# Kernel optimization log

Hardware: AMD Instinct MI355X
Metric: run time of the kernel (lower is better)

Reference implementation:

```python
import jax, jax.numpy as jnp
import numpy as np

T = 100.0  # temperature, from init_kwargs
B = 4096
D = 128
NUM_CLASSES = 10


def setup_inputs() -> dict:
    key = jax.random.key(0)
    kx, ky = jax.random.split(key)
    x = jax.random.normal(kx, (B, D), dtype=jnp.float32)
    y = jax.random.randint(ky, (B,), 0, NUM_CLASSES, dtype=jnp.int64)
    return {"x": x, "y": y}


def reference(x, y):
    # Pairwise squared Euclidean distances: dist[i,j] = ||x_i - x_j||^2
    sq = jnp.sum(x * x, axis=1)                      # [b]
    dist = sq[:, None] + sq[None, :] - 2.0 * (x @ x.T)  # [b, b]
    dist = jnp.maximum(dist, 0.0)                    # clamp fp error; diag -> 0

    e = jnp.exp(-dist / T)                           # [b, b]; e[i,i] = 1

    b = x.shape[0]
    same = (y[:, None] == y[None, :])                # same-label mask
    not_self = ~jnp.eye(b, dtype=bool)

    # numerator: sum over j != i with y[j] == y[i]
    num = jnp.sum(jnp.where(same & not_self, e, 0.0), axis=1)  # [b]
    # denominator: sum over ALL j, including j == i (exp(0) = 1), as in the
    # original loop where the denominator accumulates unconditionally
    den = jnp.sum(e, axis=1)                         # [b]

    return jnp.mean(-jnp.log(num / den))
```

## Files before the change

kernel.cpp:

```cpp
#include <hip/hip_runtime.h>
#include <hip/hip_bf16.h>

#define NB 4096

typedef short v8s __attribute__((ext_vector_type(8)));
typedef float v4f __attribute__((ext_vector_type(4)));


__global__ __launch_bounds__(256) void prep_kernel(const float* __restrict__ x,
        float* __restrict__ sq, unsigned short* __restrict__ xb,
        float* __restrict__ out) {
    int tid = threadIdx.x;
    int row = blockIdx.x * 8 + (tid >> 5);
    int lane = tid & 31;
    const float4* xg = (const float4*)x;
    float4 v = xg[row * 32 + lane];
    __hip_bfloat16 h0 = __float2bfloat16(v.x), h1 = __float2bfloat16(v.y);
    __hip_bfloat16 h2 = __float2bfloat16(v.z), h3 = __float2bfloat16(v.w);
    ushort4 u4;
    u4.x = *(unsigned short*)&h0; u4.y = *(unsigned short*)&h1;
    u4.z = *(unsigned short*)&h2; u4.w = *(unsigned short*)&h3;
    ((ushort4*)xb)[row * 32 + lane] = u4;
    float f0 = __bfloat162float(h0), f1 = __bfloat162float(h1);
    float f2 = __bfloat162float(h2), f3 = __bfloat162float(h3);
    float s = f0 * f0 + f1 * f1 + f2 * f2 + f3 * f3;
    #pragma unroll
    for (int off = 16; off > 0; off >>= 1) s += __shfl_down(s, off);
    if (lane == 0) sq[row] = s;
    if (blockIdx.x == 0 && tid == 0) out[0] = 0.f;
}

__global__ __launch_bounds__(256) void snn_mfma(const unsigned short* __restrict__ xb,
        const int* __restrict__ y, const float* __restrict__ sqg,
        float2* __restrict__ part) {
    __shared__ __align__(16) union {
        unsigned short tiles[2 * 128 * 136];
        float part[2 * 128 * 34];
    } sm;
    __shared__ float sqi[128], sqj[128];
    __shared__ int yi[128], yj[128];
    float2* partC = (float2*)&sm.part[2 * 128 * 34];

    const int tid = threadIdx.x;
    const int wave = tid >> 6;
    const int lane = tid & 63;
    const int wm = wave >> 1;
    const int wn = wave & 1;
    const int lr = lane & 15;
    const int q  = lane >> 4;

    int t = blockIdx.x;
    int by = (int)((sqrtf(8.0f * (float)t + 1.0f) - 1.0f) * 0.5f);
    if (by * (by + 1) / 2 > t) --by;
    if ((by + 1) * (by + 2) / 2 <= t) ++by;
    int bx = t - by * (by + 1) / 2;
    const int i0 = bx * 128;
    const int j0 = by * 128;
    const bool offdiag = (bx != by);

    unsigned short* At = sm.tiles;
    unsigned short* Bt = sm.tiles + 128 * 136;
    const v8s* xg = (const v8s*)xb;

    #pragma unroll
    for (int r = 0; r < 8; ++r) {
        int c = r * 256 + tid;
        int row = c >> 4, cc = c & 15;
        *(v8s*)&At[row * 136 + cc * 8] = xg[(i0 + row) * 16 + cc];
        *(v8s*)&Bt[row * 136 + cc * 8] = xg[(j0 + row) * 16 + cc];
    }
    if (tid < 128) { sqi[tid] = sqg[i0 + tid]; yi[tid] = y[i0 + tid]; }
    else { sqj[tid - 128] = sqg[j0 + tid - 128]; yj[tid - 128] = y[j0 + tid - 128]; }
    __syncthreads();

    v4f acc[4][4];
    #pragma unroll
    for (int mt = 0; mt < 4; ++mt)
        #pragma unroll
        for (int nt = 0; nt < 4; ++nt)
            #pragma unroll
            for (int r = 0; r < 4; ++r) acc[mt][nt][r] = 0.f;

    #pragma unroll
    for (int kk = 0; kk < 4; ++kk) {
        v8s af[4], bf[4];
        #pragma unroll
        for (int mt = 0; mt < 4; ++mt)
            af[mt] = *(const v8s*)&At[(wm * 64 + mt * 16 + lr) * 136 + kk * 32 + q * 8];
        #pragma unroll
        for (int nt = 0; nt < 4; ++nt)
            bf[nt] = *(const v8s*)&Bt[(wn * 64 + nt * 16 + lr) * 136 + kk * 32 + q * 8];
        #pragma unroll
        for (int mt = 0; mt < 4; ++mt)
            #pragma unroll
            for (int nt = 0; nt < 4; ++nt)
                acc[mt][nt] = __builtin_amdgcn_mfma_f32_16x16x32_bf16(
                    af[mt], bf[nt], acc[mt][nt], 0, 0, 0);
    }

    __syncthreads();

    float sqj_r[4]; int yj_r[4], jg[4];
    #pragma unroll
    for (int nt = 0; nt < 4; ++nt) {
        int jc = wn * 64 + nt * 16 + lr;
        sqj_r[nt] = sqj[jc]; yj_r[nt] = yj[jc]; jg[nt] = j0 + jc;
    }
    float colN[4] = {0.f, 0.f, 0.f, 0.f};
    float colD[4] = {0.f, 0.f, 0.f, 0.f};

    #pragma unroll
    for (int mt = 0; mt < 4; ++mt) {
        #pragma unroll
        for (int r = 0; r < 4; ++r) {
            int rloc = wm * 64 + mt * 16 + q * 4 + r;
            float si = sqi[rloc]; int yir = yi[rloc]; int ig = i0 + rloc;
            float n = 0.f, d = 0.f;
            #pragma unroll
            for (int nt = 0; nt < 4; ++nt) {
                float dist = fmaxf(si + sqj_r[nt] - 2.f * acc[mt][nt][r], 0.f);
                float e = __builtin_amdgcn_exp2f(dist * -0.014426950408889634f);
                d += e;
                bool ok = (yir == yj_r[nt]) && (ig != jg[nt]);
                float ne = ok ? e : 0.f;
                n += ne;
                colN[nt] += ne;
                colD[nt] += e;
            }
            *(float2*)&sm.part[((wn * 128 + rloc) * 17 + lr) * 2] = make_float2(n, d);
        }
    }
    if (offdiag) {
        #pragma unroll
        for (int nt = 0; nt < 4; ++nt) {
            float cn = colN[nt], cd = colD[nt];
            cn += __shfl_xor(cn, 16); cd += __shfl_xor(cd, 16);
            cn += __shfl_xor(cn, 32); cd += __shfl_xor(cd, 32);
            if (q == 0) partC[wm * 128 + wn * 64 + nt * 16 + lr] = make_float2(cn, cd);
        }
    }
    __syncthreads();

    {
        int row = tid >> 1, h = tid & 1;
        const float2* p = (const float2*)&sm.part[(h * 128 + row) * 34];
        float sn = 0.f, sd = 0.f;
        #pragma unroll
        for (int c = 0; c < 16; ++c) { float2 v = p[c]; sn += v.x; sd += v.y; }
        sn += __shfl_down(sn, 1); sd += __shfl_down(sd, 1);
        if (h == 0) part[(i0 + row) * 32 + by] = make_float2(sn, sd);
    }
    if (offdiag && tid < 128) {
        float2 a = partC[tid], b = partC[128 + tid];
        part[(j0 + tid) * 32 + bx] = make_float2(a.x + b.x, a.y + b.y);
    }
}

__global__ __launch_bounds__(256) void snn_final(const float2* __restrict__ part,
        float* __restrict__ out) {
    __shared__ float wsum[4];
    int row = blockIdx.x * 256 + threadIdx.x;
    const float4* p = (const float4*)&part[row * 32];
    float n = 0.f, d = 0.f;
    #pragma unroll
    for (int c = 0; c < 16; ++c) {
        float4 v = p[c];
        n += v.x + v.z; d += v.y + v.w;
    }
    float l = __logf(d) - __logf(n);
    #pragma unroll
    for (int off = 32; off > 0; off >>= 1) l += __shfl_down(l, off);
    int wid = threadIdx.x >> 6;
    if ((threadIdx.x & 63) == 0) wsum[wid] = l;
    __syncthreads();
    if (threadIdx.x == 0) {
        float s = wsum[0] + wsum[1] + wsum[2] + wsum[3];
        atomicAdd(out, s * (1.0f / NB));
    }
}

extern "C" void kernel_launch(void* const* d_in, const int* in_sizes, int n_in,
                              void* d_out, int out_size, void* d_ws, size_t ws_size,
                              hipStream_t stream) {
    const float* x = (const float*)d_in[0];
    const int*   y = (const int*)d_in[1];
    float* out = (float*)d_out;
    float2* part = (float2*)d_ws;
    float* sq = (float*)((char*)d_ws + (1 << 20));
    unsigned short* xb = (unsigned short*)((char*)d_ws + (1 << 20) + (16 << 10));

    prep_kernel<<<NB / 8, 256, 0, stream>>>(x, sq, xb, out);
    snn_mfma<<<528, 256, 0, stream>>>(xb, y, sq, part);
    snn_final<<<NB / 256, 256, 0, stream>>>(part, out);
}
```

Baseline: 72.34 us.

## Stage bf16 slabs via global_load_lds double buffering with k-major layout

The prep kernel now writes the bf16 copy of x in a k-chunk-major transposed layout. The MFMA kernel streams A/B k-slabs straight into LDS with global_load_lds, double-buffered so the next slab loads while the current one is multiplied. Row partial sums are now reduced with wave shuffles instead of a padded LDS scratch, which shrinks shared memory. A minimum-occupancy hint is added to launch bounds. This adds per-k barriers, and correctness relies on those barriers waiting for the async LDS loads.

```diff
diff --git a/kernel.cpp b/kernel.cpp
--- a/kernel.cpp
+++ b/kernel.cpp
@@ -7,8 +7,14 @@
 typedef float v4f __attribute__((ext_vector_type(4)));
 
 
+__device__ __forceinline__ void dma16(const unsigned short* g, unsigned short* l) {
+    __builtin_amdgcn_global_load_lds(
+        (const __attribute__((address_space(1))) unsigned int*)g,
+        (__attribute__((address_space(3))) unsigned int*)l, 16, 0, 0);
+}
+
 __global__ __launch_bounds__(256) void prep_kernel(const float* __restrict__ x,
-        float* __restrict__ sq, unsigned short* __restrict__ xb,
+        float* __restrict__ sq, unsigned short* __restrict__ xbT,
         float* __restrict__ out) {
     int tid = threadIdx.x;
     int row = blockIdx.x * 8 + (tid >> 5);
@@ -20,7 +26,8 @@
     ushort4 u4;
     u4.x = *(unsigned short*)&h0; u4.y = *(unsigned short*)&h1;
     u4.z = *(unsigned short*)&h2; u4.w = *(unsigned short*)&h3;
-    ((ushort4*)xb)[row * 32 + lane] = u4;
+    int c = lane >> 1, half = lane & 1;
+    *(ushort4*)&xbT[((size_t)c * 4096 + row) * 8 + half * 4] = u4;
     float f0 = __bfloat162float(h0), f1 = __bfloat162float(h1);
     float f2 = __bfloat162float(h2), f3 = __bfloat162float(h3);
     float s = f0 * f0 + f1 * f1 + f2 * f2 + f3 * f3;
@@ -30,22 +37,21 @@
     if (blockIdx.x == 0 && tid == 0) out[0] = 0.f;
 }
 
-__global__ __launch_bounds__(256) void snn_mfma(const unsigned short* __restrict__ xb,
+__global__ __launch_bounds__(256, 4) void snn_mfma(const unsigned short* __restrict__ xbT,
         const int* __restrict__ y, const float* __restrict__ sqg,
         float2* __restrict__ part) {
     __shared__ __align__(16) union {
-        unsigned short tiles[2 * 128 * 136];
-        float part[2 * 128 * 34];
+        unsigned short slab[2][2][4][128][8];
+        float2 red[4][128];
     } sm;
     __shared__ float sqi[128], sqj[128];
     __shared__ int yi[128], yj[128];
-    float2* partC = (float2*)&sm.part[2 * 128 * 34];
 
     const int tid = threadIdx.x;
-    const int wave = tid >> 6;
+    const int w    = tid >> 6;
     const int lane = tid & 63;
-    const int wm = wave >> 1;
-    const int wn = wave & 1;
+    const int wm = w >> 1;
+    const int wn = w & 1;
     const int lr = lane & 15;
     const int q  = lane >> 4;
 
@@ -58,20 +64,21 @@
     const int j0 = by * 128;
     const bool offdiag = (bx != by);
 
-    unsigned short* At = sm.tiles;
-    unsigned short* Bt = sm.tiles + 128 * 136;
-    const v8s* xg = (const v8s*)xb;
-
-    #pragma unroll
-    for (int r = 0; r < 8; ++r) {
-        int c = r * 256 + tid;
-        int row = c >> 4, cc = c & 15;
-        *(v8s*)&At[row * 136 + cc * 8] = xg[(i0 + row) * 16 + cc];
-        *(v8s*)&Bt[row * 136 + cc * 8] = xg[(j0 + row) * 16 + cc];
-    }
+    #define STAGE(buf, kk) do {                                                  \
+        int c_ = (kk) * 4 + w;                                                   \
+        const unsigned short* gA_ = xbT + ((size_t)(c_ * 4096 + i0) + lane) * 8; \
+        const unsigned short* gB_ = xbT + ((size_t)(c_ * 4096 + j0) + lane) * 8; \
+        unsigned short* lA_ = &sm.slab[buf][0][w][0][0];                         \
+        unsigned short* lB_ = &sm.slab[buf][1][w][0][0];                         \
+        dma16(gA_,          lA_);                                                \
+        dma16(gA_ + 64 * 8, lA_ + 64 * 8);                                       \
+        dma16(gB_,          lB_);                                                \
+        dma16(gB_ + 64 * 8, lB_ + 64 * 8);                                       \
+    } while (0)
+
+    STAGE(0, 0);
     if (tid < 128) { sqi[tid] = sqg[i0 + tid]; yi[tid] = y[i0 + tid]; }
     else { sqj[tid - 128] = sqg[j0 + tid - 128]; yj[tid - 128] = y[j0 + tid - 128]; }
-    __syncthreads();
 
     v4f acc[4][4];
     #pragma unroll
@@ -83,13 +90,16 @@
 
     #pragma unroll
     for (int kk = 0; kk < 4; ++kk) {
+        __syncthreads();
+        const int buf = kk & 1;
         v8s af[4], bf[4];
         #pragma unroll
         for (int mt = 0; mt < 4; ++mt)
-            af[mt] = *(const v8s*)&At[(wm * 64 + mt * 16 + lr) * 136 + kk * 32 + q * 8];
+            af[mt] = *(const v8s*)&sm.slab[buf][0][q][wm * 64 + mt * 16 + lr][0];
         #pragma unroll
         for (int nt = 0; nt < 4; ++nt)
-            bf[nt] = *(const v8s*)&Bt[(wn * 64 + nt * 16 + lr) * 136 + kk * 32 + q * 8];
+            bf[nt] = *(const v8s*)&sm.slab[buf][1][q][wn * 64 + nt * 16 + lr][0];
+        if (kk < 3) STAGE(buf ^ 1, kk + 1);
         #pragma unroll
         for (int mt = 0; mt < 4; ++mt)
             #pragma unroll
@@ -97,8 +107,6 @@
                 acc[mt][nt] = __builtin_amdgcn_mfma_f32_16x16x32_bf16(
                     af[mt], bf[nt], acc[mt][nt], 0, 0, 0);
     }
-
-    __syncthreads();
 
     float sqj_r[4]; int yj_r[4], jg[4];
     #pragma unroll
@@ -127,7 +135,11 @@
                 colN[nt] += ne;
                 colD[nt] += e;
             }
-            *(float2*)&sm.part[((wn * 128 + rloc) * 17 + lr) * 2] = make_float2(n, d);
+            n += __shfl_xor(n, 1); d += __shfl_xor(d, 1);
+            n += __shfl_xor(n, 2); d += __shfl_xor(d, 2);
+            n += __shfl_xor(n, 4); d += __shfl_xor(d, 4);
+            n += __shfl_xor(n, 8); d += __shfl_xor(d, 8);
+            if (lr == 0) sm.red[wn][rloc] = make_float2(n, d);
         }
     }
     if (offdiag) {
@@ -136,23 +148,18 @@
             float cn = colN[nt], cd = colD[nt];
             cn += __shfl_xor(cn, 16); cd += __shfl_xor(cd, 16);
             cn += __shfl_xor(cn, 32); cd += __shfl_xor(cd, 32);
-            if (q == 0) partC[wm * 128 + wn * 64 + nt * 16 + lr] = make_float2(cn, cd);
+            if (q == 0) sm.red[2 + wm][wn * 64 + nt * 16 + lr] = make_float2(cn, cd);
         }
     }
     __syncthreads();
 
-    {
-        int row = tid >> 1, h = tid & 1;
-        const float2* p = (const float2*)&sm.part[(h * 128 + row) * 34];
-        float sn = 0.f, sd = 0.f;
-        #pragma unroll
-        for (int c = 0; c < 16; ++c) { float2 v = p[c]; sn += v.x; sd += v.y; }
-        sn += __shfl_down(sn, 1); sd += __shfl_down(sd, 1);
-        if (h == 0) part[(i0 + row) * 32 + by] = make_float2(sn, sd);
-    }
-    if (offdiag && tid < 128) {
-        float2 a = partC[tid], b = partC[128 + tid];
-        part[(j0 + tid) * 32 + bx] = make_float2(a.x + b.x, a.y + b.y);
+    if (tid < 128) {
+        float2 a = sm.red[0][tid], b = sm.red[1][tid];
+        part[(i0 + tid) * 32 + by] = make_float2(a.x + b.x, a.y + b.y);
+    } else if (offdiag) {
+        int cc = tid - 128;
+        float2 a = sm.red[2][cc], b = sm.red[3][cc];
+        part[(j0 + cc) * 32 + bx] = make_float2(a.x + b.x, a.y + b.y);
     }
 }
 
@@ -187,9 +194,9 @@
     float* out = (float*)d_out;
     float2* part = (float2*)d_ws;
     float* sq = (float*)((char*)d_ws + (1 << 20));
-    unsigned short* xb = (unsigned short*)((char*)d_ws + (1 << 20) + (16 << 10));
-
-    prep_kernel<<<NB / 8, 256, 0, stream>>>(x, sq, xb, out);
-    snn_mfma<<<528, 256, 0, stream>>>(xb, y, sq, part);
+    unsigned short* xbT = (unsigned short*)((char*)d_ws + (1 << 20) + (16 << 10));
+
+    prep_kernel<<<NB / 8, 256, 0, stream>>>(x, sq, xbT, out);
+    snn_mfma<<<528, 256, 0, stream>>>(xbT, y, sq, part);
     snn_final<<<NB / 256, 256, 0, stream>>>(part, out);
 }
```

Result: slower. 80.88 us (+11.8%).

## Drop symmetric triangle tiling for full grid with 512-thread blocks

Applied to the files above, without the earlier changes.

Replaces the triangular 528-block schedule, which reused each off-diagonal tile for both row and column sums, with a full 32x32 grid of tiles that each compute row sums only. Blocks grow to 8 waves, each owning a 32x64 sub-tile, and the shared-memory union and column reductions give way to shuffle-based row reductions. The epilogue folds the distance and scale into one fma plus a min before exp2. This roughly doubles the MFMA and exp work in exchange for more parallelism, higher occupancy and a simpler epilogue.

```diff
diff --git a/kernel.cpp b/kernel.cpp
--- a/kernel.cpp
+++ b/kernel.cpp
@@ -30,52 +30,41 @@
     if (blockIdx.x == 0 && tid == 0) out[0] = 0.f;
 }
 
-__global__ __launch_bounds__(256) void snn_mfma(const unsigned short* __restrict__ xb,
+__global__ __launch_bounds__(512, 4) void snn_mfma(const unsigned short* __restrict__ xb,
         const int* __restrict__ y, const float* __restrict__ sqg,
         float2* __restrict__ part) {
-    __shared__ __align__(16) union {
-        unsigned short tiles[2 * 128 * 136];
-        float part[2 * 128 * 34];
-    } sm;
+    __shared__ __align__(16) unsigned short At[128 * 136];
+    __shared__ __align__(16) unsigned short Bt[128 * 136];
+    __shared__ float2 red[2][128];
     __shared__ float sqi[128], sqj[128];
     __shared__ int yi[128], yj[128];
-    float2* partC = (float2*)&sm.part[2 * 128 * 34];
 
     const int tid = threadIdx.x;
-    const int wave = tid >> 6;
+    const int w    = tid >> 6;
     const int lane = tid & 63;
-    const int wm = wave >> 1;
-    const int wn = wave & 1;
+    const int wm = w >> 1;
+    const int wn = w & 1;
     const int lr = lane & 15;
     const int q  = lane >> 4;
+    const int i0 = blockIdx.x * 128;
+    const int j0 = blockIdx.y * 128;
 
-    int t = blockIdx.x;
-    int by = (int)((sqrtf(8.0f * (float)t + 1.0f) - 1.0f) * 0.5f);
-    if (by * (by + 1) / 2 > t) --by;
-    if ((by + 1) * (by + 2) / 2 <= t) ++by;
-    int bx = t - by * (by + 1) / 2;
-    const int i0 = bx * 128;
-    const int j0 = by * 128;
-    const bool offdiag = (bx != by);
-
-    unsigned short* At = sm.tiles;
-    unsigned short* Bt = sm.tiles + 128 * 136;
     const v8s* xg = (const v8s*)xb;
-
     #pragma unroll
-    for (int r = 0; r < 8; ++r) {
-        int c = r * 256 + tid;
+    for (int it = 0; it < 4; ++it) {
+        int c = it * 512 + tid;
         int row = c >> 4, cc = c & 15;
         *(v8s*)&At[row * 136 + cc * 8] = xg[(i0 + row) * 16 + cc];
         *(v8s*)&Bt[row * 136 + cc * 8] = xg[(j0 + row) * 16 + cc];
     }
-    if (tid < 128) { sqi[tid] = sqg[i0 + tid]; yi[tid] = y[i0 + tid]; }
-    else { sqj[tid - 128] = sqg[j0 + tid - 128]; yj[tid - 128] = y[j0 + tid - 128]; }
+    if (tid < 128)      { sqi[tid] = sqg[i0 + tid];       yi[tid] = y[i0 + tid]; }
+    else if (tid < 256) { sqj[tid - 128] = sqg[j0 + tid - 128];
+                          yj[tid - 128] = y[j0 + tid - 128]; }
     __syncthreads();
 
-    v4f acc[4][4];
+    v4f acc[2][4];
     #pragma unroll
-    for (int mt = 0; mt < 4; ++mt)
+    for (int mt = 0; mt < 2; ++mt)
         #pragma unroll
         for (int nt = 0; nt < 4; ++nt)
             #pragma unroll
@@ -83,76 +72,57 @@
 
     #pragma unroll
     for (int kk = 0; kk < 4; ++kk) {
-        v8s af[4], bf[4];
+        v8s af[2], bf[4];
         #pragma unroll
-        for (int mt = 0; mt < 4; ++mt)
-            af[mt] = *(const v8s*)&At[(wm * 64 + mt * 16 + lr) * 136 + kk * 32 + q * 8];
+        for (int mt = 0; mt < 2; ++mt)
+            af[mt] = *(const v8s*)&At[(wm * 32 + mt * 16 + lr) * 136 + kk * 32 + q * 8];
         #pragma unroll
         for (int nt = 0; nt < 4; ++nt)
             bf[nt] = *(const v8s*)&Bt[(wn * 64 + nt * 16 + lr) * 136 + kk * 32 + q * 8];
         #pragma unroll
-        for (int mt = 0; mt < 4; ++mt)
+        for (int mt = 0; mt < 2; ++mt)
             #pragma unroll
             for (int nt = 0; nt < 4; ++nt)
                 acc[mt][nt] = __builtin_amdgcn_mfma_f32_16x16x32_bf16(
                     af[mt], bf[nt], acc[mt][nt], 0, 0, 0);
     }
 
-    __syncthreads();
-
-    float sqj_r[4]; int yj_r[4], jg[4];
+    const float c1 = 0.014426950408889634f;
+    const float c2 = 0.028853900817778936f;
+    float bj[4]; int yj_r[4], jg[4];
     #pragma unroll
     for (int nt = 0; nt < 4; ++nt) {
         int jc = wn * 64 + nt * 16 + lr;
-        sqj_r[nt] = sqj[jc]; yj_r[nt] = yj[jc]; jg[nt] = j0 + jc;
+        bj[nt] = -c1 * sqj[jc]; yj_r[nt] = yj[jc]; jg[nt] = j0 + jc;
     }
-    float colN[4] = {0.f, 0.f, 0.f, 0.f};
-    float colD[4] = {0.f, 0.f, 0.f, 0.f};
-
     #pragma unroll
-    for (int mt = 0; mt < 4; ++mt) {
+    for (int mt = 0; mt < 2; ++mt) {
         #pragma unroll
         for (int r = 0; r < 4; ++r) {
-            int rloc = wm * 64 + mt * 16 + q * 4 + r;
-            float si = sqi[rloc]; int yir = yi[rloc]; int ig = i0 + rloc;
+            int rloc = wm * 32 + mt * 16 + q * 4 + r;
+            float bi = -c1 * sqi[rloc];
+            int yir = yi[rloc], ig = i0 + rloc;
             float n = 0.f, d = 0.f;
             #pragma unroll
             for (int nt = 0; nt < 4; ++nt) {
-                float dist = fmaxf(si + sqj_r[nt] - 2.f * acc[mt][nt][r], 0.f);
-                float e = __builtin_amdgcn_exp2f(dist * -0.014426950408889634f);
+                float arg = fminf(0.f, fmaf(acc[mt][nt][r], c2, bi + bj[nt]));
+                float e = __builtin_amdgcn_exp2f(arg);
                 d += e;
                 bool ok = (yir == yj_r[nt]) && (ig != jg[nt]);
-                float ne = ok ? e : 0.f;
-                n += ne;
-                colN[nt] += ne;
-                colD[nt] += e;
+                n += ok ? e : 0.f;
             }
-            *(float2*)&sm.part[((wn * 128 + rloc) * 17 + lr) * 2] = make_float2(n, d);
-        }
-    }
-    if (offdiag) {
-        #pragma unroll
-        for (int nt = 0; nt < 4; ++nt) {
-            float cn = colN[nt], cd = colD[nt];
-            cn += __shfl_xor(cn, 16); cd += __shfl_xor(cd, 16);
-            cn += __shfl_xor(cn, 32); cd += __shfl_xor(cd, 32);
-            if (q == 0) partC[wm * 128 + wn * 64 + nt * 16 + lr] = make_float2(cn, cd);
+            n += __shfl_xor(n, 1); d += __shfl_xor(d, 1);
+            n += __shfl_xor(n, 2); d += __shfl_xor(d, 2);
+            n += __shfl_xor(n, 4); d += __shfl_xor(d, 4);
+            n += __shfl_xor(n, 8); d += __shfl_xor(d, 8);
+            if (lr == 0) red[wn][rloc] = make_float2(n, d);
         }
     }
     __syncthreads();
 
-    {
-        int row = tid >> 1, h = tid & 1;
-        const float2* p = (const float2*)&sm.part[(h * 128 + row) * 34];
-        float sn = 0.f, sd = 0.f;
-        #pragma unroll
-        for (int c = 0; c < 16; ++c) { float2 v = p[c]; sn += v.x; sd += v.y; }
-        sn += __shfl_down(sn, 1); sd += __shfl_down(sd, 1);
-        if (h == 0) part[(i0 + row) * 32 + by] = make_float2(sn, sd);
-    }
-    if (offdiag && tid < 128) {
-        float2 a = partC[tid], b = partC[128 + tid];
-        part[(j0 + tid) * 32 + bx] = make_float2(a.x + b.x, a.y + b.y);
+    if (tid < 128) {
+        float2 a = red[0][tid], b = red[1][tid];
+        part[(i0 + tid) * 32 + blockIdx.y] = make_float2(a.x + b.x, a.y + b.y);
     }
 }
 
@@ -190,6 +160,7 @@
     unsigned short* xb = (unsigned short*)((char*)d_ws + (1 << 20) + (16 << 10));
 
     prep_kernel<<<NB / 8, 256, 0, stream>>>(x, sq, xb, out);
-    snn_mfma<<<528, 256, 0, stream>>>(xb, y, sq, part);
+    dim3 grid(NB / 128, NB / 128);
+    snn_mfma<<<grid, 512, 0, stream>>>(xb, y, sq, part);
     snn_final<<<NB / 256, 256, 0, stream>>>(part, out);
 }
```

After: 76.17 us. +5.3%, slower.
